# Kernel optimization log

Hardware: AMD Instinct MI355X
Metric: run time of the kernel (lower is better)

Reference implementation:

```python
import jax, jax.numpy as jnp
import numpy as np

B, N, C, H = 16, 577, 384, 6
ONE_DIM = 24
RPD = 2 * ONE_DIM - 1  # 47
NUM_CLS = 1
HEAD_DIM = C // H
SCALE = HEAD_DIM ** -0.5


def _build_rel_pos_index():
    # Faithful to the torch loop: tmp[dy - y + off, dx - x + off] with
    # torch's negative-index wraparound -> modulo RPD.
    off = ONE_DIM // 2
    qy = np.repeat(np.arange(ONE_DIM), ONE_DIM)  # (Np,) y of each query patch
    qx = np.tile(np.arange(ONE_DIM), ONE_DIM)    # (Np,) x of each query patch
    ky, kx = qy, qx                              # key patches use same grid
    ry = (ky[None, :] - qy[:, None] + off) % RPD
    rx = (kx[None, :] - qx[:, None] + off) % RPD
    return jnp.asarray(ry * RPD + rx, dtype=jnp.int32)  # (Np, Np)


def setup_inputs() -> dict:
    key = jax.random.key(0)
    k = jax.random.split(key, 6)
    x = jax.random.normal(k[0], (B, N, C), dtype=jnp.float32)
    qkv_w = jax.random.normal(k[1], (3 * C, C), dtype=jnp.float32) * 0.02
    qkv_b = jnp.zeros((3 * C,), dtype=jnp.float32)
    proj_w = jax.random.normal(k[2], (C, C), dtype=jnp.float32) * 0.02
    proj_b = jnp.zeros((C,), dtype=jnp.float32)
    rel_pos = jax.random.normal(k[3], (H, RPD * RPD), dtype=jnp.float32) * 0.02
    mask = jax.random.randint(k[4], (B, N, N), 0, 2, dtype=jnp.int32)
    return {
        "x": x, "qkv_w": qkv_w, "qkv_b": qkv_b,
        "proj_w": proj_w, "proj_b": proj_b, "rel_pos": rel_pos,
        "rel_pos_index": _build_rel_pos_index(),
        "mask": mask, "patch_attn": 1,
    }


def reference(x, qkv_w, qkv_b, proj_w, proj_b, rel_pos, rel_pos_index, mask, patch_attn):
    # qkv projection: torch Linear -> x @ W^T + b
    qkv = x @ qkv_w.T + qkv_b                               # (B, N, 3C)
    qkv = qkv.reshape(B, N, 3, H, HEAD_DIM).transpose(2, 0, 3, 1, 4)
    q, k, v = qkv[0], qkv[1], qkv[2]                        # (B, H, N, hd)

    attn = jnp.einsum("bhqd,bhkd->bhqk", q, k) * SCALE      # (B, H, N, N)

    if patch_attn:
        # gather per-head relative-position bias for patch tokens
        bias = rel_pos[:, rel_pos_index]                    # (H, Np, Np)
        attn = attn.at[:, :, NUM_CLS:, NUM_CLS:].add(bias)

    neg = jnp.finfo(attn.dtype).min
    attn = jnp.where(mask[:, None, :, :] == 0, neg, attn)   # broadcast over heads

    attn = jax.nn.softmax(attn, axis=-1)
    out = jnp.einsum("bhqk,bhkd->bhqd", attn, v)            # (B, H, N, hd)
    out = out.transpose(0, 2, 1, 3).reshape(B, N, C)
    out = out @ proj_w.T + proj_b
    return out
```

## Files before the change

kernel.cpp:

```cpp
#include <hip/hip_runtime.h>
#include <float.h>
#include <math.h>

#define NB 16
#define NN 577
#define NC 384
#define NH 6
#define ND 64
#define RPD2 2209
#define MTOT 9232
#define MPAD 9344
#define SCALE_ 0.125f
#define NEGBIG -3.0e38f
#define BSTRIDE 580
#define NKPAD 640

typedef __attribute__((ext_vector_type(8))) short bf16x8;
typedef __attribute__((ext_vector_type(4))) float f32x4;
typedef unsigned short u16;

#define MFMA16(a, b, c) __builtin_amdgcn_mfma_f32_16x16x32_bf16(a, b, c, 0, 0, 0)

#define SQA 3932160ull
#define OFF_QH 0ull
#define OFF_QL SQA
#define OFF_KH (2ull * SQA)
#define OFF_KL (3ull * SQA)
#define OFF_VTH (4ull * SQA)
#define OFF_VTL (5ull * SQA)
#define OFF_XH (6ull * SQA)
#define OFF_XL (6ull * SQA + 3588096ull)
#define OFF_WQH (6ull * SQA + 2ull * 3588096ull)
#define OFF_WQL (OFF_WQH + 442368ull)
#define OFF_WPH (OFF_WQL + 442368ull)
#define OFF_WPL (OFF_WPH + 147456ull)
#define OFF_BT  (OFF_WPL + 147456ull)
#define OFF_PM  (OFF_BT + 2007960ull)

static __device__ __forceinline__ u16 f2bf(float f) {
  unsigned u = __float_as_uint(f);
  u += 0x7fff + ((u >> 16) & 1);
  return (u16)(u >> 16);
}
static __device__ __forceinline__ float bf2f(u16 h) {
  return __uint_as_float((unsigned)h << 16);
}
static __device__ __forceinline__ void split2(float v, u16& hi, u16& lo) {
  hi = f2bf(v);
  lo = f2bf(v - bf2f(hi));
}
static __device__ __forceinline__ void gload16(const void* g, void* l) {
  __builtin_amdgcn_global_load_lds(
      (const __attribute__((address_space(1))) void*)g,
      (__attribute__((address_space(3))) void*)l, 16, 0, 0);
}

__global__ __launch_bounds__(256) void split_inputs_k(
    const float* __restrict__ x, const float* __restrict__ wq,
    const float* __restrict__ wp, u16* __restrict__ ws)
{
  const int q = blockIdx.x * 256 + threadIdx.x;
  float4 v = {0.f, 0.f, 0.f, 0.f};
  u16 *dh, *dl;
  if (q < 897024) {
    if (q < 886272) v = ((const float4*)x)[q];
    dh = ws + OFF_XH + 4ull * q;
    dl = ws + OFF_XL + 4ull * q;
  } else if (q < 1007616) {
    int t = q - 897024;
    v = ((const float4*)wq)[t];
    dh = ws + OFF_WQH + 4ull * t;
    dl = ws + OFF_WQL + 4ull * t;
  } else {
    int t = q - 1007616;
    v = ((const float4*)wp)[t];
    dh = ws + OFF_WPH + 4ull * t;
    dl = ws + OFF_WPL + 4ull * t;
  }
  ushort4 hh, ll;
  split2(v.x, hh.x, ll.x);
  split2(v.y, hh.y, ll.y);
  split2(v.z, hh.z, ll.z);
  split2(v.w, hh.w, ll.w);
  *(ushort4*)dh = hh;
  *(ushort4*)dl = ll;
}

__global__ __launch_bounds__(256) void pack_mask_k(const int* __restrict__ mask,
                                                   unsigned* __restrict__ pm)
{
  const int wid = (blockIdx.x * 256 + threadIdx.x) >> 6;
  const int lane = threadIdx.x & 63;
  if (wid >= MTOT) return;
  const int* mr = mask + (size_t)wid * NN;
#pragma unroll
  for (int c = 0; c < 10; ++c) {
    int k = c * 64 + lane;
    int v = (k < NN) ? mr[k] : 0;
    unsigned long long bal = __ballot(v != 0);
    if (lane == 0) pm[wid * 20 + 2 * c] = (unsigned)bal;
    if (lane == 1) pm[wid * 20 + 2 * c + 1] = (unsigned)(bal >> 32);
  }
}

__global__ __launch_bounds__(256) void bias_build_k(
    const float* __restrict__ rel_pos, const int* __restrict__ rel_idx,
    const int* __restrict__ patch, u16* __restrict__ tbl)
{
  const int q = blockIdx.x;
  const int h = blockIdx.y;
  const int pa = *patch;
  u16* row = tbl + ((size_t)h * NN + q) * BSTRIDE;
  for (int kk = threadIdx.x; kk < BSTRIDE; kk += 256) {
    float v = 0.f;
    if (pa && q >= 1 && kk >= 1 && kk < NN)
      v = rel_pos[h * RPD2 + rel_idx[(q - 1) * 576 + (kk - 1)]];
    row[kk] = f2bf(v);
  }
}

__global__ __launch_bounds__(256, 2) void qkv_mfma_k(
    const u16* __restrict__ Xh, const u16* __restrict__ Xl,
    const u16* __restrict__ Wh, const u16* __restrict__ Wl,
    const float* __restrict__ bias, u16* __restrict__ ws)
{
  __shared__ u16 Ash[2][4096], Asl[2][4096];
  __shared__ u16 Bsh[2][4096], Bsl[2][4096];

  const int tid = threadIdx.x;
  const int w = tid >> 6, l = tid & 63, lq = l & 15, lg = l >> 4;
  const int wm = (w >> 1) * 64, wn = (w & 1) * 64;
  const int mb = blockIdx.x * 128;
  const int rb = blockIdx.y * 128;
  const int r0 = rb + wn;
  const int soff = (l >> 2) * 384 + (l & 3) * 8;

#define STAGE_AB(k0_, bf_)                                                   \
  {                                                                          \
    _Pragma("unroll")                                                        \
    for (int j = 0; j < 2; ++j) {                                            \
      const int tr = 32 * w + 16 * j;                                        \
      const size_t ga = (size_t)(mb + tr) * 384 + (k0_) + soff;              \
      const size_t gb = (size_t)(rb + tr) * 384 + (k0_) + soff;              \
      gload16(&Xh[ga], &Ash[bf_][tr * 32]);                                  \
      gload16(&Xl[ga], &Asl[bf_][tr * 32]);                                  \
      gload16(&Wh[gb], &Bsh[bf_][tr * 32]);                                  \
      gload16(&Wl[gb], &Bsl[bf_][tr * 32]);                                  \
    }                                                                        \
  }

  STAGE_AB(0, 0);

  f32x4 acc[4][4];
#pragma unroll
  for (int nt = 0; nt < 4; ++nt) {
    float bv = bias[r0 + 16 * nt + lq];
#pragma unroll
    for (int mt = 0; mt < 4; ++mt) acc[mt][nt] = (f32x4){bv, bv, bv, bv};
  }

  for (int k0 = 0; k0 < 384; k0 += 32) {
    const int bfb = (k0 >> 5) & 1;
    __syncthreads();
    if (k0 < 352) STAGE_AB(k0 + 32, bfb ^ 1);

    bf16x8 bhf[4], blf[4];
#pragma unroll
    for (int nt = 0; nt < 4; ++nt) {
      bhf[nt] = *(const bf16x8*)&Bsh[bfb][(wn + 16 * nt + lq) * 32 + 8 * lg];
      blf[nt] = *(const bf16x8*)&Bsl[bfb][(wn + 16 * nt + lq) * 32 + 8 * lg];
    }
#pragma unroll
    for (int mt = 0; mt < 4; ++mt) {
      bf16x8 ah = *(const bf16x8*)&Ash[bfb][(wm + 16 * mt + lq) * 32 + 8 * lg];
      bf16x8 al = *(const bf16x8*)&Asl[bfb][(wm + 16 * mt + lq) * 32 + 8 * lg];
#pragma unroll
      for (int nt = 0; nt < 4; ++nt) {
        acc[mt][nt] = MFMA16(ah, bhf[nt], acc[mt][nt]);
        acc[mt][nt] = MFMA16(ah, blf[nt], acc[mt][nt]);
        acc[mt][nt] = MFMA16(al, bhf[nt], acc[mt][nt]);
      }
    }
  }
#undef STAGE_AB

  const int comp = rb / 384;
  const int h = ((rb % 384) + wn) >> 6;
#pragma unroll
  for (int mt = 0; mt < 4; ++mt)
#pragma unroll
    for (int r = 0; r < 4; ++r) {
      int m = mb + wm + 16 * mt + 4 * lg + r;
      if (m >= MTOT) continue;
      int bb = m / NN, nn = m - bb * NN;
      int bh = bb * NH + h;
#pragma unroll
      for (int nt = 0; nt < 4; ++nt) {
        int d = 16 * nt + lq;
        float v = acc[mt][nt][r];
        u16 hi, lo;
        if (comp == 0) {
          v *= SCALE_;
          split2(v, hi, lo);
          size_t a = ((size_t)bh * NKPAD + nn) * 64 + d;
          ws[OFF_QH + a] = hi;
          ws[OFF_QL + a] = lo;
        } else if (comp == 1) {
          split2(v, hi, lo);
          size_t a = ((size_t)bh * NKPAD + nn) * 64 + d;
          ws[OFF_KH + a] = hi;
          ws[OFF_KL + a] = lo;
        } else {
          split2(v, hi, lo);
          size_t a = ((size_t)bh * 64 + d) * NKPAD + nn;
          ws[OFF_VTH + a] = hi;
          ws[OFF_VTL + a] = lo;
        }
      }
    }
}

__global__ __launch_bounds__(256, 2) void attn_k(
    const u16* __restrict__ Qh, const u16* __restrict__ Ql,
    const u16* __restrict__ Kh, const u16* __restrict__ Kl,
    const u16* __restrict__ Vth, const u16* __restrict__ Vtl,
    const u16* __restrict__ btbl, const unsigned* __restrict__ pm,
    u16* __restrict__ Oh, u16* __restrict__ Ol)
{
  __shared__ u16 Kth[2][4096], Ktl[2][4096];
  __shared__ u16 Vsh[2][4096], Vsl[2][4096];
  __shared__ u16 Ph[4][2048];

  const int tid = threadIdx.x;
  const int w = tid >> 6, l = tid & 63, lq = l & 15, lg = l >> 4;
  const int q0 = blockIdx.x * 128;
  const int h = blockIdx.y, b = blockIdx.z;
  const int bh = b * NH + h;
  const int qr0 = q0 + 32 * w + lq;
  const int qr1 = qr0 + 16;
  const int swz = (lq & 7) << 3;
  const int ln8 = l >> 3, lc8 = l & 7;
  const int koff = ln8 * 64 + ((lc8 ^ ln8) << 3);
  const int voff = ln8 * NKPAD + ((lc8 ^ ln8) << 3);

#define STAGE(ch, bf)                                                        \
  {                                                                          \
    const int kb_ = (ch) * 64;                                               \
    const size_t kgb = ((size_t)bh * NKPAD + kb_ + 16 * w) * 64 + koff;      \
    const size_t vgb = ((size_t)bh * 64 + 16 * w) * NKPAD + kb_ + voff;      \
    gload16(&Kh[kgb],              &Kth[bf][(16 * w) * 64]);                 \
    gload16(&Kh[kgb + 512],        &Kth[bf][(16 * w + 8) * 64]);             \
    gload16(&Kl[kgb],              &Ktl[bf][(16 * w) * 64]);                 \
    gload16(&Kl[kgb + 512],        &Ktl[bf][(16 * w + 8) * 64]);             \
    gload16(&Vth[vgb],             &Vsh[bf][(16 * w) * 64]);                 \
    gload16(&Vth[vgb + 8 * NKPAD], &Vsh[bf][(16 * w + 8) * 64]);             \
    gload16(&Vtl[vgb],             &Vsl[bf][(16 * w) * 64]);                 \
    gload16(&Vtl[vgb + 8 * NKPAD], &Vsl[bf][(16 * w + 8) * 64]);             \
  }

  STAGE(0, 0);

  const size_t qb0 = ((size_t)bh * NKPAD + qr0) * 64 + 8 * lg;
  const size_t qb1 = ((size_t)bh * NKPAD + qr1) * 64 + 8 * lg;
  bf16x8 q0h[2], q0l[2], q1h[2], q1l[2];
  q0h[0] = *(const bf16x8*)&Qh[qb0];
  q0h[1] = *(const bf16x8*)&Qh[qb0 + 32];
  q0l[0] = *(const bf16x8*)&Ql[qb0];
  q0l[1] = *(const bf16x8*)&Ql[qb0 + 32];
  q1h[0] = *(const bf16x8*)&Qh[qb1];
  q1h[1] = *(const bf16x8*)&Qh[qb1 + 32];
  q1l[0] = *(const bf16x8*)&Ql[qb1];
  q1l[1] = *(const bf16x8*)&Ql[qb1 + 32];

  const int gq0 = (qr0 < NN) ? qr0 : NN - 1;
  const int gq1 = (qr1 < NN) ? qr1 : NN - 1;
  const bool qv0 = qr0 < NN, qv1 = qr1 < NN;
  const unsigned* pmrow0 = pm + ((size_t)b * NN + gq0) * 20;
  const unsigned* pmrow1 = pm + ((size_t)b * NN + gq1) * 20;
  const size_t brow0 = ((size_t)h * NN + gq0) * BSTRIDE;
  const size_t brow1 = ((size_t)h * NN + gq1) * BSTRIDE;

  uint2 cM0, cM1, nM0, nM1;
  uint2 cB0[4], cB1[4], nB0[4], nB1[4];
  cM0 = *(const uint2*)&pmrow0[0];
  cM1 = *(const uint2*)&pmrow1[0];
#pragma unroll
  for (int t = 0; t < 4; ++t) {
    int kkb = 16 * t + 4 * lg;
    cB0[t] = (qv0 && kkb <= 576) ? *(const uint2*)&btbl[brow0 + kkb]
                                 : make_uint2(0u, 0u);
    cB1[t] = (qv1 && kkb <= 576) ? *(const uint2*)&btbl[brow1 + kkb]
                                 : make_uint2(0u, 0u);
  }

  float m_reg0 = NEGBIG, l_reg0 = 0.f;
  float m_reg1 = NEGBIG, l_reg1 = 0.f;
  f32x4 accO0[4] = {}, accO1[4] = {};

  for (int ch = 0; ch < 10; ++ch) {
    const int bf = ch & 1;
    __syncthreads();
    if (ch < 9) {
      nM0 = *(const uint2*)&pmrow0[2 * (ch + 1)];
      nM1 = *(const uint2*)&pmrow1[2 * (ch + 1)];
      const int kb2 = (ch + 1) * 64;
#pragma unroll
      for (int t = 0; t < 4; ++t) {
        int kkb = kb2 + 16 * t + 4 * lg;
        nB0[t] = (qv0 && kkb <= 576) ? *(const uint2*)&btbl[brow0 + kkb]
                                     : make_uint2(0u, 0u);
        nB1[t] = (qv1 && kkb <= 576) ? *(const uint2*)&btbl[brow1 + kkb]
                                     : make_uint2(0u, 0u);
      }
      STAGE(ch + 1, bf ^ 1);
    }

    unsigned long long m64_0 = (unsigned long long)cM0.x |
                               ((unsigned long long)cM0.y << 32);
    unsigned long long m64_1 = (unsigned long long)cM1.x |
                               ((unsigned long long)cM1.y << 32);

    float sv0[4][4], sv1[4][4];
    __builtin_amdgcn_s_setprio(1);
#pragma unroll
    for (int t = 0; t < 4; ++t) {
      f32x4 a0, a1;
      a0[0] = bf2f((u16)(cB0[t].x & 0xffff));
      a0[1] = bf2f((u16)(cB0[t].x >> 16));
      a0[2] = bf2f((u16)(cB0[t].y & 0xffff));
      a0[3] = bf2f((u16)(cB0[t].y >> 16));
      a1[0] = bf2f((u16)(cB1[t].x & 0xffff));
      a1[1] = bf2f((u16)(cB1[t].x >> 16));
      a1[2] = bf2f((u16)(cB1[t].y & 0xffff));
      a1[3] = bf2f((u16)(cB1[t].y >> 16));
      const int ar = (16 * t + lq) * 64;
#pragma unroll
      for (int ks = 0; ks < 2; ++ks) {
        const int c = (8 * lg + 32 * ks) ^ swz;
        bf16x8 ah = *(const bf16x8*)&Kth[bf][ar + c];
        bf16x8 al = *(const bf16x8*)&Ktl[bf][ar + c];
        a0 = MFMA16(ah, q0h[ks], a0);
        a0 = MFMA16(ah, q0l[ks], a0);
        a0 = MFMA16(al, q0h[ks], a0);
        a1 = MFMA16(ah, q1h[ks], a1);
        a1 = MFMA16(ah, q1l[ks], a1);
        a1 = MFMA16(al, q1h[ks], a1);
      }
#pragma unroll
      for (int r = 0; r < 4; ++r) { sv0[t][r] = a0[r]; sv1[t][r] = a1[r]; }
    }
    __builtin_amdgcn_s_setprio(0);

    {
      float cmax = NEGBIG;
#pragma unroll
      for (int t = 0; t < 4; ++t)
#pragma unroll
        for (int r = 0; r < 4; ++r) {
          int kl = 16 * t + 4 * lg + r;
          float s = ((m64_0 >> kl) & 1ull) ? sv0[t][r] : NEGBIG;
          sv0[t][r] = s;
          cmax = fmaxf(cmax, s);
        }
      cmax = fmaxf(cmax, __shfl_xor(cmax, 16));
      cmax = fmaxf(cmax, __shfl_xor(cmax, 32));
      float m_new = fmaxf(m_reg0, cmax);
      float fx = __expf(m_reg0 - m_new);
      float csum = 0.f;
#pragma unroll
      for (int t = 0; t < 4; ++t) {
        float e0 = __expf(sv0[t][0] - m_new);
        float e1 = __expf(sv0[t][1] - m_new);
        float e2 = __expf(sv0[t][2] - m_new);
        float e3 = __expf(sv0[t][3] - m_new);
        csum += e0 + e1 + e2 + e3;
        ushort4 ph;
        ph.x = f2bf(e0); ph.y = f2bf(e1); ph.z = f2bf(e2); ph.w = f2bf(e3);
        *(ushort4*)&Ph[w][lq * 64 + ((16 * t + 4 * lg) ^ swz)] = ph;
      }
      csum += __shfl_xor(csum, 16);
      csum += __shfl_xor(csum, 32);
      l_reg0 = l_reg0 * fx + csum;
      m_reg0 = m_new;
      float fxr[4];
#pragma unroll
      for (int r = 0; r < 4; ++r) fxr[r] = __shfl(fx, 4 * lg + r);
#pragma unroll
      for (int t = 0; t < 4; ++t) {
        accO0[t][0] *= fxr[0]; accO0[t][1] *= fxr[1];
        accO0[t][2] *= fxr[2]; accO0[t][3] *= fxr[3];
      }
    }
    {
      float cmax = NEGBIG;
#pragma unroll
      for (int t = 0; t < 4; ++t)
#pragma unroll
        for (int r = 0; r < 4; ++r) {
          int kl = 16 * t + 4 * lg + r;
          float s = ((m64_1 >> kl) & 1ull) ? sv1[t][r] : NEGBIG;
          sv1[t][r] = s;
          cmax = fmaxf(cmax, s);
        }
      cmax = fmaxf(cmax, __shfl_xor(cmax, 16));
      cmax = fmaxf(cmax, __shfl_xor(cmax, 32));
      float m_new = fmaxf(m_reg1, cmax);
      float fx = __expf(m_reg1 - m_new);
      float csum = 0.f;
#pragma unroll
      for (int t = 0; t < 4; ++t) {
        float e0 = __expf(sv1[t][0] - m_new);
        float e1 = __expf(sv1[t][1] - m_new);
        float e2 = __expf(sv1[t][2] - m_new);
        float e3 = __expf(sv1[t][3] - m_new);
        csum += e0 + e1 + e2 + e3;
        ushort4 ph;
        ph.x = f2bf(e0); ph.y = f2bf(e1); ph.z = f2bf(e2); ph.w = f2bf(e3);
        *(ushort4*)&Ph[w][(16 + lq) * 64 + ((16 * t + 4 * lg) ^ swz)] = ph;
      }
      csum += __shfl_xor(csum, 16);
      csum += __shfl_xor(csum, 32);
      l_reg1 = l_reg1 * fx + csum;
      m_reg1 = m_new;
      float fxr[4];
#pragma unroll
      for (int r = 0; r < 4; ++r) fxr[r] = __shfl(fx, 4 * lg + r);
#pragma unroll
      for (int t = 0; t < 4; ++t) {
        accO1[t][0] *= fxr[0]; accO1[t][1] *= fxr[1];
        accO1[t][2] *= fxr[2]; accO1[t][3] *= fxr[3];
      }
    }

    bf16x8 pa0[2], pa1[2];
#pragma unroll
    for (int ks = 0; ks < 2; ++ks) {
      int c = (8 * lg + 32 * ks) ^ swz;
      pa0[ks] = *(const bf16x8*)&Ph[w][lq * 64 + c];
      pa1[ks] = *(const bf16x8*)&Ph[w][(16 + lq) * 64 + c];
    }

    __builtin_amdgcn_s_setprio(1);
#pragma unroll
    for (int t = 0; t < 4; ++t) {
      const int vr = (16 * t + lq) * 64;
#pragma unroll
      for (int ks = 0; ks < 2; ++ks) {
        const int c = (8 * lg + 32 * ks) ^ swz;
        bf16x8 vh = *(const bf16x8*)&Vsh[bf][vr + c];
        bf16x8 vl = *(const bf16x8*)&Vsl[bf][vr + c];
        accO0[t] = MFMA16(pa0[ks], vh, accO0[t]);
        accO0[t] = MFMA16(pa0[ks], vl, accO0[t]);
        accO1[t] = MFMA16(pa1[ks], vh, accO1[t]);
        accO1[t] = MFMA16(pa1[ks], vl, accO1[t]);
      }
    }
    __builtin_amdgcn_s_setprio(0);

    if (ch < 9) {
      cM0 = nM0; cM1 = nM1;
#pragma unroll
      for (int t = 0; t < 4; ++t) { cB0[t] = nB0[t]; cB1[t] = nB1[t]; }
    }
  }
#undef STAGE

  float il0 = 1.f / l_reg0;
  float il1 = 1.f / l_reg1;
  float ilr0[4], ilr1[4];
#pragma unroll
  for (int r = 0; r < 4; ++r) {
    ilr0[r] = __shfl(il0, 4 * lg + r);
    ilr1[r] = __shfl(il1, 4 * lg + r);
  }
#pragma unroll
  for (int t = 0; t < 4; ++t)
#pragma unroll
    for (int r = 0; r < 4; ++r) {
      int g0 = q0 + 32 * w + 4 * lg + r;
      if (g0 < NN) {
        float v = accO0[t][r] * ilr0[r];
        u16 hi, lo;
        split2(v, hi, lo);
        size_t a = ((size_t)b * NN + g0) * NC + h * 64 + 16 * t + lq;
        Oh[a] = hi;
        Ol[a] = lo;
      }
      int g1 = g0 + 16;
      if (g1 < NN) {
        float v = accO1[t][r] * ilr1[r];
        u16 hi, lo;
        split2(v, hi, lo);
        size_t a = ((size_t)b * NN + g1) * NC + h * 64 + 16 * t + lq;
        Oh[a] = hi;
        Ol[a] = lo;
      }
    }
}

__global__ __launch_bounds__(256, 2) void proj_mfma_k(
    const u16* __restrict__ Ah, const u16* __restrict__ Al,
    const u16* __restrict__ Wh, const u16* __restrict__ Wl,
    const float* __restrict__ bias, float* __restrict__ out)
{
  __shared__ u16 Ash[2][4096], Asl[2][4096];
  __shared__ u16 Bsh[2][4096], Bsl[2][4096];

  const int tid = threadIdx.x;
  const int w = tid >> 6, l = tid & 63, lq = l & 15, lg = l >> 4;
  const int wm = (w >> 1) * 64, wn = (w & 1) * 64;
  const int mb = blockIdx.x * 128;
  const int rb = blockIdx.y * 128;
  const int r0 = rb + wn;
  const int soff = (l >> 2) * 384 + (l & 3) * 8;

#define STAGE_AB(k0_, bf_)                                                   \
  {                                                                          \
    _Pragma("unroll")                                                        \
    for (int j = 0; j < 2; ++j) {                                            \
      const int tr = 32 * w + 16 * j;                                        \
      const size_t ga = (size_t)(mb + tr) * 384 + (k0_) + soff;              \
      const size_t gb = (size_t)(rb + tr) * 384 + (k0_) + soff;              \
      gload16(&Ah[ga], &Ash[bf_][tr * 32]);                                  \
      gload16(&Al[ga], &Asl[bf_][tr * 32]);                                  \
      gload16(&Wh[gb], &Bsh[bf_][tr * 32]);                                  \
      gload16(&Wl[gb], &Bsl[bf_][tr * 32]);                                  \
    }                                                                        \
  }

  STAGE_AB(0, 0);

  f32x4 acc[4][4];
#pragma unroll
  for (int nt = 0; nt < 4; ++nt) {
    float bv = bias[r0 + 16 * nt + lq];
#pragma unroll
    for (int mt = 0; mt < 4; ++mt) acc[mt][nt] = (f32x4){bv, bv, bv, bv};
  }

  for (int k0 = 0; k0 < 384; k0 += 32) {
    const int bfb = (k0 >> 5) & 1;
    __syncthreads();
    if (k0 < 352) STAGE_AB(k0 + 32, bfb ^ 1);

    bf16x8 bhf[4], blf[4];
#pragma unroll
    for (int nt = 0; nt < 4; ++nt) {
      bhf[nt] = *(const bf16x8*)&Bsh[bfb][(wn + 16 * nt + lq) * 32 + 8 * lg];
      blf[nt] = *(const bf16x8*)&Bsl[bfb][(wn + 16 * nt + lq) * 32 + 8 * lg];
    }
#pragma unroll
    for (int mt = 0; mt < 4; ++mt) {
      bf16x8 ah = *(const bf16x8*)&Ash[bfb][(wm + 16 * mt + lq) * 32 + 8 * lg];
      bf16x8 al = *(const bf16x8*)&Asl[bfb][(wm + 16 * mt + lq) * 32 + 8 * lg];
#pragma unroll
      for (int nt = 0; nt < 4; ++nt) {
        acc[mt][nt] = MFMA16(ah, bhf[nt], acc[mt][nt]);
        acc[mt][nt] = MFMA16(ah, blf[nt], acc[mt][nt]);
        acc[mt][nt] = MFMA16(al, bhf[nt], acc[mt][nt]);
      }
    }
  }
#undef STAGE_AB

#pragma unroll
  for (int mt = 0; mt < 4; ++mt)
#pragma unroll
    for (int r = 0; r < 4; ++r) {
      int m = mb + wm + 16 * mt + 4 * lg + r;
      if (m >= MTOT) continue;
#pragma unroll
      for (int nt = 0; nt < 4; ++nt)
        out[(size_t)m * NC + r0 + 16 * nt + lq] = acc[mt][nt][r];
    }
}

extern "C" void kernel_launch(void* const* d_in, const int* in_sizes, int n_in,
                              void* d_out, int out_size, void* d_ws, size_t ws_size,
                              hipStream_t stream) {
  const float* x       = (const float*)d_in[0];
  const float* qkv_w   = (const float*)d_in[1];
  const float* qkv_b   = (const float*)d_in[2];
  const float* proj_w  = (const float*)d_in[3];
  const float* proj_b  = (const float*)d_in[4];
  const float* rel_pos = (const float*)d_in[5];
  const int*   rel_idx = (const int*)d_in[6];
  const int*   mask    = (const int*)d_in[7];
  const int*   patch   = (const int*)d_in[8];
  float* out = (float*)d_out;
  u16* W16 = (u16*)d_ws;

  unsigned* pmp = (unsigned*)(W16 + OFF_PM);
  u16* btblp = W16 + OFF_BT;

  split_inputs_k<<<4080, 256, 0, stream>>>(x, qkv_w, proj_w, W16);
  pack_mask_k<<<2308, 256, 0, stream>>>(mask, pmp);
  bias_build_k<<<dim3(NN, NH), 256, 0, stream>>>(rel_pos, rel_idx, patch, btblp);
  qkv_mfma_k<<<dim3(73, 9), 256, 0, stream>>>(
      W16 + OFF_XH, W16 + OFF_XL, W16 + OFF_WQH, W16 + OFF_WQL, qkv_b, W16);
  attn_k<<<dim3(5, NH, NB), 256, 0, stream>>>(
      W16 + OFF_QH, W16 + OFF_QL, W16 + OFF_KH, W16 + OFF_KL,
      W16 + OFF_VTH, W16 + OFF_VTL, btblp, pmp,
      W16 + OFF_XH, W16 + OFF_XL);
  proj_mfma_k<<<dim3(73, 3), 256, 0, stream>>>(
      W16 + OFF_XH, W16 + OFF_XL, W16 + OFF_WPH, W16 + OFF_WPL, proj_b, out);
}
```

Before: 164.3 us.

## Fuse prep kernels and load GEMM B operand directly into registers with prefetch

Merges the three preprocessing kernels (input split, mask packing, bias table build) into one launch, distinguished by block index ranges, to save launch gaps. In the QKV and projection GEMMs, the weight (B) tiles are no longer staged through shared memory. Each wave loads its B fragments straight from global memory into registers, prefetched one k-step ahead, while the A tiles keep a two-stage LDS pipeline with explicit waitcnt and barriers. This halves LDS use so launch bounds allow 3 blocks per CU, at the cost of more registers and uncoalesced direct global loads for B.

```diff
diff --git a/kernel.cpp b/kernel.cpp
--- a/kernel.cpp
+++ b/kernel.cpp
@@ -55,77 +55,76 @@
       (__attribute__((address_space(3))) void*)l, 16, 0, 0);
 }
 
-__global__ __launch_bounds__(256) void split_inputs_k(
+__global__ __launch_bounds__(256) void prep_k(
     const float* __restrict__ x, const float* __restrict__ wq,
-    const float* __restrict__ wp, u16* __restrict__ ws)
+    const float* __restrict__ wp, const int* __restrict__ mask,
+    const float* __restrict__ rel_pos, const int* __restrict__ rel_idx,
+    const int* __restrict__ patch, u16* __restrict__ ws)
 {
-  const int q = blockIdx.x * 256 + threadIdx.x;
-  float4 v = {0.f, 0.f, 0.f, 0.f};
-  u16 *dh, *dl;
-  if (q < 897024) {
-    if (q < 886272) v = ((const float4*)x)[q];
-    dh = ws + OFF_XH + 4ull * q;
-    dl = ws + OFF_XL + 4ull * q;
-  } else if (q < 1007616) {
-    int t = q - 897024;
-    v = ((const float4*)wq)[t];
-    dh = ws + OFF_WQH + 4ull * t;
-    dl = ws + OFF_WQL + 4ull * t;
+  const int bidx = blockIdx.x;
+  const int tid = threadIdx.x;
+
+  if (bidx < 4080) {
+    const int q = bidx * 256 + tid;
+    float4 v = {0.f, 0.f, 0.f, 0.f};
+    u16 *dh, *dl;
+    if (q < 897024) {
+      if (q < 886272) v = ((const float4*)x)[q];
+      dh = ws + OFF_XH + 4ull * q;
+      dl = ws + OFF_XL + 4ull * q;
+    } else if (q < 1007616) {
+      int t = q - 897024;
+      v = ((const float4*)wq)[t];
+      dh = ws + OFF_WQH + 4ull * t;
+      dl = ws + OFF_WQL + 4ull * t;
+    } else {
+      int t = q - 1007616;
+      v = ((const float4*)wp)[t];
+      dh = ws + OFF_WPH + 4ull * t;
+      dl = ws + OFF_WPL + 4ull * t;
+    }
+    ushort4 hh, ll;
+    split2(v.x, hh.x, ll.x);
+    split2(v.y, hh.y, ll.y);
+    split2(v.z, hh.z, ll.z);
+    split2(v.w, hh.w, ll.w);
+    *(ushort4*)dh = hh;
+    *(ushort4*)dl = ll;
+  } else if (bidx < 6388) {
+    unsigned* pm = (unsigned*)(ws + OFF_PM);
+    const int pbid = bidx - 4080;
+    const int wid = (pbid * 256 + tid) >> 6;
+    const int lane = tid & 63;
+    if (wid >= MTOT) return;
+    const int* mr = mask + (size_t)wid * NN;
+#pragma unroll
+    for (int c = 0; c < 10; ++c) {
+      int k = c * 64 + lane;
+      int v = (k < NN) ? mr[k] : 0;
+      unsigned long long bal = __ballot(v != 0);
+      if (lane == 0) pm[wid * 20 + 2 * c] = (unsigned)bal;
+      if (lane == 1) pm[wid * 20 + 2 * c + 1] = (unsigned)(bal >> 32);
+    }
   } else {
-    int t = q - 1007616;
-    v = ((const float4*)wp)[t];
-    dh = ws + OFF_WPH + 4ull * t;
-    dl = ws + OFF_WPL + 4ull * t;
-  }
-  ushort4 hh, ll;
-  split2(v.x, hh.x, ll.x);
-  split2(v.y, hh.y, ll.y);
-  split2(v.z, hh.z, ll.z);
-  split2(v.w, hh.w, ll.w);
-  *(ushort4*)dh = hh;
-  *(ushort4*)dl = ll;
-}
-
-__global__ __launch_bounds__(256) void pack_mask_k(const int* __restrict__ mask,
-                                                   unsigned* __restrict__ pm)
-{
-  const int wid = (blockIdx.x * 256 + threadIdx.x) >> 6;
-  const int lane = threadIdx.x & 63;
-  if (wid >= MTOT) return;
-  const int* mr = mask + (size_t)wid * NN;
-#pragma unroll
-  for (int c = 0; c < 10; ++c) {
-    int k = c * 64 + lane;
-    int v = (k < NN) ? mr[k] : 0;
-    unsigned long long bal = __ballot(v != 0);
-    if (lane == 0) pm[wid * 20 + 2 * c] = (unsigned)bal;
-    if (lane == 1) pm[wid * 20 + 2 * c + 1] = (unsigned)(bal >> 32);
-  }
-}
-
-__global__ __launch_bounds__(256) void bias_build_k(
-    const float* __restrict__ rel_pos, const int* __restrict__ rel_idx,
-    const int* __restrict__ patch, u16* __restrict__ tbl)
-{
-  const int q = blockIdx.x;
-  const int h = blockIdx.y;
-  const int pa = *patch;
-  u16* row = tbl + ((size_t)h * NN + q) * BSTRIDE;
-  for (int kk = threadIdx.x; kk < BSTRIDE; kk += 256) {
-    float v = 0.f;
-    if (pa && q >= 1 && kk >= 1 && kk < NN)
-      v = rel_pos[h * RPD2 + rel_idx[(q - 1) * 576 + (kk - 1)]];
-    row[kk] = f2bf(v);
-  }
-}
-
-__global__ __launch_bounds__(256, 2) void qkv_mfma_k(
+    const int f = bidx - 6388;
+    const int q = f % NN, h = f / NN;
+    const int pa = *patch;
+    u16* row = ws + OFF_BT + ((size_t)h * NN + q) * BSTRIDE;
+    for (int kk = tid; kk < BSTRIDE; kk += 256) {
+      float v = 0.f;
+      if (pa && q >= 1 && kk >= 1 && kk < NN)
+        v = rel_pos[h * RPD2 + rel_idx[(q - 1) * 576 + (kk - 1)]];
+      row[kk] = f2bf(v);
+    }
+  }
+}
+
+__global__ __launch_bounds__(256, 3) void qkv_mfma_k(
     const u16* __restrict__ Xh, const u16* __restrict__ Xl,
     const u16* __restrict__ Wh, const u16* __restrict__ Wl,
     const float* __restrict__ bias, u16* __restrict__ ws)
 {
   __shared__ u16 Ash[2][4096], Asl[2][4096];
-  __shared__ u16 Bsh[2][4096], Bsl[2][4096];
 
   const int tid = threadIdx.x;
   const int w = tid >> 6, l = tid & 63, lq = l & 15, lg = l >> 4;
@@ -135,21 +134,46 @@
   const int r0 = rb + wn;
   const int soff = (l >> 2) * 384 + (l & 3) * 8;
 
-#define STAGE_AB(k0_, bf_)                                                   \
+#define STAGE_A(k0_, bf_)                                                    \
   {                                                                          \
     _Pragma("unroll")                                                        \
     for (int j = 0; j < 2; ++j) {                                            \
       const int tr = 32 * w + 16 * j;                                        \
       const size_t ga = (size_t)(mb + tr) * 384 + (k0_) + soff;              \
-      const size_t gb = (size_t)(rb + tr) * 384 + (k0_) + soff;              \
       gload16(&Xh[ga], &Ash[bf_][tr * 32]);                                  \
       gload16(&Xl[ga], &Asl[bf_][tr * 32]);                                  \
-      gload16(&Wh[gb], &Bsh[bf_][tr * 32]);                                  \
-      gload16(&Wl[gb], &Bsl[bf_][tr * 32]);                                  \
     }                                                                        \
   }
 
-  STAGE_AB(0, 0);
+  const size_t brow = (size_t)(r0 + lq) * 384 + 8 * lg;
+#define BLOAD(k0_, BH_, BL_)                                                 \
+  {                                                                          \
+    _Pragma("unroll")                                                        \
+    for (int nt = 0; nt < 4; ++nt) {                                         \
+      BH_[nt] = *(const bf16x8*)&Wh[brow + (size_t)(16 * nt) * 384 + (k0_)]; \
+      BL_[nt] = *(const bf16x8*)&Wl[brow + (size_t)(16 * nt) * 384 + (k0_)]; \
+    }                                                                        \
+  }
+
+#define COMPUTE(bf_)                                                         \
+  {                                                                          \
+    _Pragma("unroll")                                                        \
+    for (int mt = 0; mt < 4; ++mt) {                                         \
+      bf16x8 ah = *(const bf16x8*)&Ash[bf_][(wm + 16 * mt + lq) * 32 + 8 * lg]; \
+      bf16x8 al = *(const bf16x8*)&Asl[bf_][(wm + 16 * mt + lq) * 32 + 8 * lg]; \
+      _Pragma("unroll")                                                      \
+      for (int nt = 0; nt < 4; ++nt) {                                       \
+        acc[mt][nt] = MFMA16(ah, bhf[nt], acc[mt][nt]);                      \
+        acc[mt][nt] = MFMA16(ah, blf[nt], acc[mt][nt]);                      \
+        acc[mt][nt] = MFMA16(al, bhf[nt], acc[mt][nt]);                      \
+      }                                                                      \
+    }                                                                        \
+  }
+
+  bf16x8 bhf[4], blf[4], nbh[4], nbl[4];
+  BLOAD(0, bhf, blf);
+  STAGE_A(0, 0);
+  STAGE_A(32, 1);
 
   f32x4 acc[4][4];
 #pragma unroll
@@ -159,30 +183,30 @@
     for (int mt = 0; mt < 4; ++mt) acc[mt][nt] = (f32x4){bv, bv, bv, bv};
   }
 
-  for (int k0 = 0; k0 < 384; k0 += 32) {
-    const int bfb = (k0 >> 5) & 1;
-    __syncthreads();
-    if (k0 < 352) STAGE_AB(k0 + 32, bfb ^ 1);
-
-    bf16x8 bhf[4], blf[4];
-#pragma unroll
-    for (int nt = 0; nt < 4; ++nt) {
-      bhf[nt] = *(const bf16x8*)&Bsh[bfb][(wn + 16 * nt + lq) * 32 + 8 * lg];
-      blf[nt] = *(const bf16x8*)&Bsl[bfb][(wn + 16 * nt + lq) * 32 + 8 * lg];
-    }
-#pragma unroll
-    for (int mt = 0; mt < 4; ++mt) {
-      bf16x8 ah = *(const bf16x8*)&Ash[bfb][(wm + 16 * mt + lq) * 32 + 8 * lg];
-      bf16x8 al = *(const bf16x8*)&Asl[bfb][(wm + 16 * mt + lq) * 32 + 8 * lg];
-#pragma unroll
-      for (int nt = 0; nt < 4; ++nt) {
-        acc[mt][nt] = MFMA16(ah, bhf[nt], acc[mt][nt]);
-        acc[mt][nt] = MFMA16(ah, blf[nt], acc[mt][nt]);
-        acc[mt][nt] = MFMA16(al, bhf[nt], acc[mt][nt]);
-      }
-    }
-  }
-#undef STAGE_AB
+  for (int k = 0; k < 11; ++k) {
+    asm volatile("s_waitcnt vmcnt(4)" ::: "memory");
+    __builtin_amdgcn_sched_barrier(0);
+    __builtin_amdgcn_s_barrier();
+    __builtin_amdgcn_sched_barrier(0);
+    const int bfb = k & 1;
+    COMPUTE(bfb);
+    __builtin_amdgcn_sched_barrier(0);
+    __builtin_amdgcn_s_barrier();
+    __builtin_amdgcn_sched_barrier(0);
+    BLOAD(32 * (k + 1), nbh, nbl);
+    if (k < 10) STAGE_A(32 * (k + 2), bfb);
+#pragma unroll
+    for (int nt = 0; nt < 4; ++nt) { bhf[nt] = nbh[nt]; blf[nt] = nbl[nt]; }
+  }
+  asm volatile("s_waitcnt vmcnt(0)" ::: "memory");
+  __builtin_amdgcn_sched_barrier(0);
+  __builtin_amdgcn_s_barrier();
+  __builtin_amdgcn_sched_barrier(0);
+  COMPUTE(1);
+
+#undef COMPUTE
+#undef BLOAD
+#undef STAGE_A
 
   const int comp = rb / 384;
   const int h = ((rb % 384) + wn) >> 6;
@@ -498,13 +522,12 @@
     }
 }
 
-__global__ __launch_bounds__(256, 2) void proj_mfma_k(
+__global__ __launch_bounds__(256, 3) void proj_mfma_k(
     const u16* __restrict__ Ah, const u16* __restrict__ Al,
     const u16* __restrict__ Wh, const u16* __restrict__ Wl,
     const float* __restrict__ bias, float* __restrict__ out)
 {
   __shared__ u16 Ash[2][4096], Asl[2][4096];
-  __shared__ u16 Bsh[2][4096], Bsl[2][4096];
 
   const int tid = threadIdx.x;
   const int w = tid >> 6, l = tid & 63, lq = l & 15, lg = l >> 4;
@@ -514,21 +537,46 @@
   const int r0 = rb + wn;
   const int soff = (l >> 2) * 384 + (l & 3) * 8;
 
-#define STAGE_AB(k0_, bf_)                                                   \
+#define STAGE_A(k0_, bf_)                                                    \
   {                                                                          \
     _Pragma("unroll")                                                        \
     for (int j = 0; j < 2; ++j) {                                            \
       const int tr = 32 * w + 16 * j;                                        \
       const size_t ga = (size_t)(mb + tr) * 384 + (k0_) + soff;              \
-      const size_t gb = (size_t)(rb + tr) * 384 + (k0_) + soff;              \
       gload16(&Ah[ga], &Ash[bf_][tr * 32]);                                  \
       gload16(&Al[ga], &Asl[bf_][tr * 32]);                                  \
-      gload16(&Wh[gb], &Bsh[bf_][tr * 32]);                                  \
-      gload16(&Wl[gb], &Bsl[bf_][tr * 32]);                                  \
     }                                                                        \
   }
 
-  STAGE_AB(0, 0);
+  const size_t brow = (size_t)(r0 + lq) * 384 + 8 * lg;
+#define BLOAD(k0_, BH_, BL_)                                                 \
+  {                                                                          \
+    _Pragma("unroll")                                                        \
+    for (int nt = 0; nt < 4; ++nt) {                                         \
+      BH_[nt] = *(const bf16x8*)&Wh[brow + (size_t)(16 * nt) * 384 + (k0_)]; \
+      BL_[nt] = *(const bf16x8*)&Wl[brow + (size_t)(16 * nt) * 384 + (k0_)]; \
+    }                                                                        \
+  }
+
+#define COMPUTE(bf_)                                                         \
+  {                                                                          \
+    _Pragma("unroll")                                                        \
+    for (int mt = 0; mt < 4; ++mt) {                                         \
+      bf16x8 ah = *(const bf16x8*)&Ash[bf_][(wm + 16 * mt + lq) * 32 + 8 * lg]; \
+      bf16x8 al = *(const bf16x8*)&Asl[bf_][(wm + 16 * mt + lq) * 32 + 8 * lg]; \
+      _Pragma("unroll")                                                      \
+      for (int nt = 0; nt < 4; ++nt) {                                       \
+        acc[mt][nt] = MFMA16(ah, bhf[nt], acc[mt][nt]);                      \
+        acc[mt][nt] = MFMA16(ah, blf[nt], acc[mt][nt]);                      \
+        acc[mt][nt] = MFMA16(al, bhf[nt], acc[mt][nt]);                      \
+      }                                                                      \
+    }                                                                        \
+  }
+
+  bf16x8 bhf[4], blf[4], nbh[4], nbl[4];
+  BLOAD(0, bhf, blf);
+  STAGE_A(0, 0);
+  STAGE_A(32, 1);
 
   f32x4 acc[4][4];
 #pragma unroll
@@ -538,30 +586,30 @@
     for (int mt = 0; mt < 4; ++mt) acc[mt][nt] = (f32x4){bv, bv, bv, bv};
   }
 
-  for (int k0 = 0; k0 < 384; k0 += 32) {
-    const int bfb = (k0 >> 5) & 1;
-    __syncthreads();
-    if (k0 < 352) STAGE_AB(k0 + 32, bfb ^ 1);
-
-    bf16x8 bhf[4], blf[4];
-#pragma unroll
-    for (int nt = 0; nt < 4; ++nt) {
-      bhf[nt] = *(const bf16x8*)&Bsh[bfb][(wn + 16 * nt + lq) * 32 + 8 * lg];
-      blf[nt] = *(const bf16x8*)&Bsl[bfb][(wn + 16 * nt + lq) * 32 + 8 * lg];
-    }
-#pragma unroll
-    for (int mt = 0; mt < 4; ++mt) {
-      bf16x8 ah = *(const bf16x8*)&Ash[bfb][(wm + 16 * mt + lq) * 32 + 8 * lg];
-      bf16x8 al = *(const bf16x8*)&Asl[bfb][(wm + 16 * mt + lq) * 32 + 8 * lg];
-#pragma unroll
-      for (int nt = 0; nt < 4; ++nt) {
-        acc[mt][nt] = MFMA16(ah, bhf[nt], acc[mt][nt]);
-        acc[mt][nt] = MFMA16(ah, blf[nt], acc[mt][nt]);
-        acc[mt][nt] = MFMA16(al, bhf[nt], acc[mt][nt]);
-      }
-    }
-  }
-#undef STAGE_AB
+  for (int k = 0; k < 11; ++k) {
+    asm volatile("s_waitcnt vmcnt(4)" ::: "memory");
+    __builtin_amdgcn_sched_barrier(0);
+    __builtin_amdgcn_s_barrier();
+    __builtin_amdgcn_sched_barrier(0);
+    const int bfb = k & 1;
+    COMPUTE(bfb);
+    __builtin_amdgcn_sched_barrier(0);
+    __builtin_amdgcn_s_barrier();
+    __builtin_amdgcn_sched_barrier(0);
+    BLOAD(32 * (k + 1), nbh, nbl);
+    if (k < 10) STAGE_A(32 * (k + 2), bfb);
+#pragma unroll
+    for (int nt = 0; nt < 4; ++nt) { bhf[nt] = nbh[nt]; blf[nt] = nbl[nt]; }
+  }
+  asm volatile("s_waitcnt vmcnt(0)" ::: "memory");
+  __builtin_amdgcn_sched_barrier(0);
+  __builtin_amdgcn_s_barrier();
+  __builtin_amdgcn_sched_barrier(0);
+  COMPUTE(1);
+
+#undef COMPUTE
+#undef BLOAD
+#undef STAGE_A
 
 #pragma unroll
   for (int mt = 0; mt < 4; ++mt)
@@ -593,9 +641,8 @@
   unsigned* pmp = (unsigned*)(W16 + OFF_PM);
   u16* btblp = W16 + OFF_BT;
 
-  split_inputs_k<<<4080, 256, 0, stream>>>(x, qkv_w, proj_w, W16);
-  pack_mask_k<<<2308, 256, 0, stream>>>(mask, pmp);
-  bias_build_k<<<dim3(NN, NH), 256, 0, stream>>>(rel_pos, rel_idx, patch, btblp);
+  prep_k<<<9850, 256, 0, stream>>>(x, qkv_w, proj_w, mask, rel_pos, rel_idx,
+                                   patch, W16);
   qkv_mfma_k<<<dim3(73, 9), 256, 0, stream>>>(
       W16 + OFF_XH, W16 + OFF_XL, W16 + OFF_WQH, W16 + OFF_WQL, qkv_b, W16);
   attn_k<<<dim3(5, NH, NB), 256, 0, stream>>>(
```

Measured after the change: 160.5 us. -2.3%, faster.
